# Optimization experiments

Hardware: AMD Instinct MI355X
Metric: run time of the kernel (lower is better)

The kernel has to match this reference:

```python
import jax, jax.numpy as jnp
import numpy as np

N = 50000
E = 800000
IN_F, HID, OUT_F = 512, 256, 64
KEEP = 0.5  # Dropout(0.5)


def setup_inputs() -> dict:
    key = jax.random.key(0)
    ks = jax.random.split(key, 7)
    X = jax.random.normal(ks[0], (N, IN_F), dtype=jnp.float32)
    # Xavier-uniform-style init for the two layer weights
    lim1 = float(np.sqrt(6.0 / (IN_F + HID)))
    lim2 = float(np.sqrt(6.0 / (HID + OUT_F)))
    W1 = jax.random.uniform(ks[1], (IN_F, HID), jnp.float32, -lim1, lim1)
    W2 = jax.random.uniform(ks[2], (HID, OUT_F), jnp.float32, -lim2, lim2)
    a_row = jnp.sort(jax.random.randint(ks[3], (E,), 0, N)).astype(jnp.int64)
    a_col = jax.random.randint(ks[4], (E,), 0, N).astype(jnp.int64)
    a_val = jax.random.uniform(ks[5], (E,), jnp.float32)
    drop_mask = jax.random.randint(ks[6], (N, HID), 0, 2).astype(jnp.int32)
    return {"X": X, "W1": W1, "W2": W2, "a_row": a_row, "a_col": a_col,
            "a_val": a_val, "drop_mask": drop_mask}


def _spmm(a_row, a_col, a_val, dense):
    # A @ dense where A is [N, N] sparse in COO form: gather + weighted segment-sum
    msgs = a_val[:, None] * dense[a_col]          # [E, d]
    return jax.ops.segment_sum(msgs, a_row, num_segments=N)


def reference(X, W1, W2, a_row, a_col, a_val, drop_mask):
    # layer 1: feature transform + neighbor aggregation
    h = _spmm(a_row, a_col, a_val, X @ W1)        # [N, HID]
    h = jax.nn.relu(h)
    h = h * drop_mask.astype(h.dtype) * (1.0 / KEEP)  # Dropout(0.5), train mode
    # layer 2
    out = _spmm(a_row, a_col, a_val, h @ W2)      # [N, OUT_F]
    return jax.nn.log_softmax(out, axis=1)
```

## Files before the change

### kernel.cpp

```cpp
#include <hip/hip_runtime.h>
#include <hip/hip_bf16.h>
#include <math.h>

#define NN   50000
#define EE   800000
#define INF  512
#define HIDF 256
#define OUTF 64
#define MTILES (NN/16)

using short8 = __attribute__((ext_vector_type(8))) short;
using short4v = __attribute__((ext_vector_type(4))) short;
using f32x4  = __attribute__((ext_vector_type(4))) float;

static __device__ __forceinline__ short f2bf(float f){
  unsigned u = __builtin_bit_cast(unsigned, f);
  u += 0x7fff + ((u >> 16) & 1);
  return (short)(u >> 16);
}
static __device__ __forceinline__ float bf2f(short s){
  unsigned u = ((unsigned)(unsigned short)s) << 16;
  return __builtin_bit_cast(float, u);
}

__global__ void k_rowptr(const int* __restrict__ a_row, int* __restrict__ row_ptr){
  int i = blockIdx.x * blockDim.x + threadIdx.x;
  if (i > NN) return;
  int lo = 0, hi = EE;
  while (lo < hi){ int mid = (lo + hi) >> 1; if (a_row[mid] < i) lo = mid + 1; else hi = mid; }
  row_ptr[i] = lo;
}

__global__ void k_pack_w1(const float* __restrict__ W1, short* __restrict__ W1p){
  int idx = blockIdx.x * blockDim.x + threadIdx.x;
  int k = idx >> 8, col = idx & 255;
  int kk = k >> 5, k2 = k & 31;
  W1p[((kk << 8) + col) * 32 + k2] = f2bf(W1[idx]);
}

__global__ void k_transpose_bf16(const float* __restrict__ src, short* __restrict__ dst,
                                 int K, int Ncols){
  int idx = blockIdx.x * blockDim.x + threadIdx.x;
  if (idx >= K * Ncols) return;
  int k = idx / Ncols, n = idx % Ncols;
  dst[n * K + k] = f2bf(src[idx]);
}

__global__ __launch_bounds__(256) void k_gemm1(const float* __restrict__ X,
                                               const short* __restrict__ W1p,
                                               short* __restrict__ XW1b){
  __shared__ short lds[256 * 40];
  int wave = threadIdx.x >> 6, lane = threadIdx.x & 63;
  int l16 = lane & 15, quad = lane >> 4;
  int m0 = blockIdx.x * 64 + wave * 16;
  int arow_idx = min(m0 + l16, NN - 1);
  const float* arow = X + (size_t)arow_idx * INF + quad * 8;

  f32x4 acc[16];
  #pragma unroll
  for (int t = 0; t < 16; t++) acc[t] = (f32x4){0.f,0.f,0.f,0.f};

  for (int kk = 0; kk < INF/32; kk++){
    const short* chunk = W1p + kk * (256*32);
    #pragma unroll
    for (int j = 0; j < 4; j++){
      int off16 = j * 256 + threadIdx.x;
      int col = off16 >> 2, kq = threadIdx.x & 3;
      *(short8*)(lds + col * 40 + kq * 8) = *(const short8*)(chunk + off16 * 8);
    }
    __syncthreads();

    const float4* ap = (const float4*)(arow + kk * 32);
    float4 a0 = ap[0], a1 = ap[1];
    short8 af;
    af[0]=f2bf(a0.x); af[1]=f2bf(a0.y); af[2]=f2bf(a0.z); af[3]=f2bf(a0.w);
    af[4]=f2bf(a1.x); af[5]=f2bf(a1.y); af[6]=f2bf(a1.z); af[7]=f2bf(a1.w);
    #pragma unroll
    for (int nt = 0; nt < 16; nt++){
      short8 bf = *(const short8*)(lds + (nt*16 + l16) * 40 + quad * 8);
      acc[nt] = __builtin_amdgcn_mfma_f32_16x16x32_bf16(af, bf, acc[nt], 0, 0, 0);
    }
    __syncthreads();
  }
  #pragma unroll
  for (int nt = 0; nt < 16; nt++){
    int col = nt*16 + l16;
    #pragma unroll
    for (int r = 0; r < 4; r++){
      int row = m0 + quad*4 + r;
      if (row < NN) XW1b[(size_t)row * HIDF + col] = f2bf(acc[nt][r]);
    }
  }
}

__global__ __launch_bounds__(256) void k_spmm1(const int* __restrict__ row_ptr,
                                               const int* __restrict__ a_col,
                                               const float* __restrict__ a_val,
                                               const short* __restrict__ XW1b,
                                               const int* __restrict__ drop_mask,
                                               short* __restrict__ hb){
  int wave = threadIdx.x >> 6, lane = threadIdx.x & 63;
  int r = blockIdx.x * 4 + wave;
  int s = row_ptr[r], e = row_ptr[r+1];
  int g = lane >> 5;
  int c8 = lane & 31;
  float acc[8] = {0,0,0,0,0,0,0,0};

  for (int i = s + g; i < e; i += 2){
    float v = a_val[i];
    int   c = a_col[i];
    short8 x = *(const short8*)(XW1b + (size_t)c * HIDF + c8 * 8);
    #pragma unroll
    for (int j = 0; j < 8; j++) acc[j] += v * bf2f(x[j]);
  }
  #pragma unroll
  for (int j = 0; j < 8; j++) acc[j] += __shfl_xor(acc[j], 32);

  if (lane < 32){
    int4 d0 = *(const int4*)(drop_mask + (size_t)r * HIDF + c8 * 8);
    int4 d1 = *(const int4*)(drop_mask + (size_t)r * HIDF + c8 * 8 + 4);
    short8 o;
    o[0] = f2bf(fmaxf(acc[0],0.f) * (float)d0.x * 2.0f);
    o[1] = f2bf(fmaxf(acc[1],0.f) * (float)d0.y * 2.0f);
    o[2] = f2bf(fmaxf(acc[2],0.f) * (float)d0.z * 2.0f);
    o[3] = f2bf(fmaxf(acc[3],0.f) * (float)d0.w * 2.0f);
    o[4] = f2bf(fmaxf(acc[4],0.f) * (float)d1.x * 2.0f);
    o[5] = f2bf(fmaxf(acc[5],0.f) * (float)d1.y * 2.0f);
    o[6] = f2bf(fmaxf(acc[6],0.f) * (float)d1.z * 2.0f);
    o[7] = f2bf(fmaxf(acc[7],0.f) * (float)d1.w * 2.0f);
    *(short8*)(hb + (size_t)r * HIDF + c8 * 8) = o;
  }
}

__global__ __launch_bounds__(256) void k_gemm2(const short* __restrict__ A,
                                               const short* __restrict__ BT,
                                               short* __restrict__ C){
  int wave = threadIdx.x >> 6, lane = threadIdx.x & 63;
  int tile_m = blockIdx.x * 4 + wave;
  if (tile_m >= MTILES) return;
  int m0 = tile_m * 16, l16 = lane & 15, quad = lane >> 4;

  f32x4 acc[4];
  #pragma unroll
  for (int t = 0; t < 4; t++) acc[t] = (f32x4){0.f,0.f,0.f,0.f};

  const short* ar = A + (size_t)(m0 + l16) * HIDF + quad * 8;
  for (int kk = 0; kk < HIDF/32; kk++){
    short8 af = *(const short8*)(ar + kk * 32);
    #pragma unroll
    for (int nt = 0; nt < 4; nt++){
      short8 bf = *(const short8*)(BT + (size_t)(nt*16 + l16) * HIDF + kk*32 + quad*8);
      acc[nt] = __builtin_amdgcn_mfma_f32_16x16x32_bf16(af, bf, acc[nt], 0, 0, 0);
    }
  }
  #pragma unroll
  for (int nt = 0; nt < 4; nt++){
    int col = nt*16 + l16;
    #pragma unroll
    for (int r = 0; r < 4; r++)
      C[(size_t)(m0 + quad*4 + r) * OUTF + col] = f2bf(acc[nt][r]);
  }
}

__global__ __launch_bounds__(256) void k_spmm2_lsm(const int* __restrict__ row_ptr,
                                                   const int* __restrict__ a_col,
                                                   const float* __restrict__ a_val,
                                                   const short* __restrict__ HW2b,
                                                   float* __restrict__ out){
  int wave = threadIdx.x >> 6, lane = threadIdx.x & 63;
  int r = blockIdx.x * 4 + wave;
  int s = row_ptr[r], e = row_ptr[r+1];
  int g = lane >> 4;
  int c4 = lane & 15;
  float acc[4] = {0,0,0,0};

  for (int i = s + g; i < e; i += 4){
    float v = a_val[i];
    int   c = a_col[i];
    short4v x = *(const short4v*)(HW2b + (size_t)c * OUTF + c4 * 4);
    #pragma unroll
    for (int j = 0; j < 4; j++) acc[j] += v * bf2f(x[j]);
  }
  #pragma unroll
  for (int j = 0; j < 4; j++){
    acc[j] += __shfl_xor(acc[j], 16);
    acc[j] += __shfl_xor(acc[j], 32);
  }
  float m = fmaxf(fmaxf(acc[0], acc[1]), fmaxf(acc[2], acc[3]));
  #pragma unroll
  for (int o = 1; o <= 8; o <<= 1) m = fmaxf(m, __shfl_xor(m, o));
  float ssum = expf(acc[0]-m) + expf(acc[1]-m) + expf(acc[2]-m) + expf(acc[3]-m);
  #pragma unroll
  for (int o = 1; o <= 8; o <<= 1) ssum += __shfl_xor(ssum, o);
  float ls = logf(ssum);
  if (lane < 16){
    float4 o4 = { acc[0]-m-ls, acc[1]-m-ls, acc[2]-m-ls, acc[3]-m-ls };
    *(float4*)(out + (size_t)r * OUTF + c4 * 4) = o4;
  }
}

extern "C" void kernel_launch(void* const* d_in, const int* in_sizes, int n_in,
                              void* d_out, int out_size, void* d_ws, size_t ws_size,
                              hipStream_t stream) {
  const float* X      = (const float*)d_in[0];
  const float* W1     = (const float*)d_in[1];
  const float* W2     = (const float*)d_in[2];
  const int*   a_row  = (const int*)d_in[3];
  const int*   a_col  = (const int*)d_in[4];
  const float* a_val  = (const float*)d_in[5];
  const int*   drop   = (const int*)d_in[6];
  float*       out    = (float*)d_out;

  char* ws = (char*)d_ws;
  int*   row_ptr = (int*)  (ws);
  short* W1p     = (short*)(ws + 200704);
  short* W2bT    = (short*)(ws + 462848);
  short* XW1b    = (short*)(ws + 495616);
  short* hb      = (short*)(ws + 26095616);
  short* HW2b    = (short*)(ws + 51695616);

  k_rowptr<<<(NN + 1 + 255)/256, 256, 0, stream>>>(a_row, row_ptr);
  k_pack_w1<<<(INF*HIDF)/256, 256, 0, stream>>>(W1, W1p);
  k_transpose_bf16<<<(HIDF*OUTF + 255)/256, 256, 0, stream>>>(W2, W2bT, HIDF, OUTF);
  k_gemm1<<<(NN + 63)/64, 256, 0, stream>>>(X, W1p, XW1b);
  k_spmm1<<<NN/4, 256, 0, stream>>>(row_ptr, a_col, a_val, XW1b, drop, hb);
  k_gemm2<<<(MTILES + 3)/4, 256, 0, stream>>>(hb, W2bT, HW2b);
  k_spmm2_lsm<<<NN/4, 256, 0, stream>>>(row_ptr, a_col, a_val, HW2b, out);
}
```

Baseline: 358.3 us.

## Merge prep kernels, double gemm1 row tile, unroll and widen SpMM gathers

Folds the row-pointer, W1 packing and W2 transpose kernels into a single launch, which removes two kernel launches. gemm1 now has each wave compute two 16-row tiles, so every LDS load of W1 feeds twice as many MFMAs, and the X loads are issued before the barrier. Both SpMM kernels unroll the edge loop by two so more gathers are in flight; spmm1 also moves to 4 edge groups with 16 columns per lane. The cost is higher register pressure in gemm1 (twice the accumulators) and in spmm1 (16 accumulators per lane).

```diff
diff --git a/kernel.cpp b/kernel.cpp
--- a/kernel.cpp
+++ b/kernel.cpp
@@ -23,27 +23,26 @@
   return __builtin_bit_cast(float, u);
 }
 
-__global__ void k_rowptr(const int* __restrict__ a_row, int* __restrict__ row_ptr){
-  int i = blockIdx.x * blockDim.x + threadIdx.x;
-  if (i > NN) return;
-  int lo = 0, hi = EE;
-  while (lo < hi){ int mid = (lo + hi) >> 1; if (a_row[mid] < i) lo = mid + 1; else hi = mid; }
-  row_ptr[i] = lo;
-}
-
-__global__ void k_pack_w1(const float* __restrict__ W1, short* __restrict__ W1p){
-  int idx = blockIdx.x * blockDim.x + threadIdx.x;
-  int k = idx >> 8, col = idx & 255;
-  int kk = k >> 5, k2 = k & 31;
-  W1p[((kk << 8) + col) * 32 + k2] = f2bf(W1[idx]);
-}
-
-__global__ void k_transpose_bf16(const float* __restrict__ src, short* __restrict__ dst,
-                                 int K, int Ncols){
-  int idx = blockIdx.x * blockDim.x + threadIdx.x;
-  if (idx >= K * Ncols) return;
-  int k = idx / Ncols, n = idx % Ncols;
-  dst[n * K + k] = f2bf(src[idx]);
+__global__ void k_prep(const int* __restrict__ a_row, int* __restrict__ row_ptr,
+                       const float* __restrict__ W1, short* __restrict__ W1p,
+                       const float* __restrict__ W2, short* __restrict__ W2bT){
+  int b = blockIdx.x, tid = threadIdx.x;
+  if (b < 196){
+    int i = b * 256 + tid;
+    if (i > NN) return;
+    int lo = 0, hi = EE;
+    while (lo < hi){ int mid = (lo + hi) >> 1; if (a_row[mid] < i) lo = mid + 1; else hi = mid; }
+    row_ptr[i] = lo;
+  } else if (b < 708){
+    int idx = (b - 196) * 256 + tid;
+    int k = idx >> 8, col = idx & 255;
+    int kk = k >> 5, k2 = k & 31;
+    W1p[((kk << 8) + col) * 32 + k2] = f2bf(W1[idx]);
+  } else {
+    int idx = (b - 708) * 256 + tid;
+    int k = idx >> 6, n = idx & 63;
+    W2bT[n * HIDF + k] = f2bf(W2[idx]);
+  }
 }
 
 __global__ __launch_bounds__(256) void k_gemm1(const float* __restrict__ X,
@@ -52,15 +51,22 @@
   __shared__ short lds[256 * 40];
   int wave = threadIdx.x >> 6, lane = threadIdx.x & 63;
   int l16 = lane & 15, quad = lane >> 4;
-  int m0 = blockIdx.x * 64 + wave * 16;
-  int arow_idx = min(m0 + l16, NN - 1);
-  const float* arow = X + (size_t)arow_idx * INF + quad * 8;
-
-  f32x4 acc[16];
-  #pragma unroll
-  for (int t = 0; t < 16; t++) acc[t] = (f32x4){0.f,0.f,0.f,0.f};
+  int m0 = blockIdx.x * 128 + wave * 32;
+  int r0 = min(m0 + l16, NN - 1);
+  int r1 = min(m0 + 16 + l16, NN - 1);
+  const float* arow0 = X + (size_t)r0 * INF + quad * 8;
+  const float* arow1 = X + (size_t)r1 * INF + quad * 8;
+
+  f32x4 acc0[16], acc1[16];
+  #pragma unroll
+  for (int t = 0; t < 16; t++){ acc0[t] = (f32x4){0.f,0.f,0.f,0.f}; acc1[t] = (f32x4){0.f,0.f,0.f,0.f}; }
 
   for (int kk = 0; kk < INF/32; kk++){
+    const float4* ap0 = (const float4*)(arow0 + kk * 32);
+    const float4* ap1 = (const float4*)(arow1 + kk * 32);
+    float4 a00 = ap0[0], a01 = ap0[1];
+    float4 a10 = ap1[0], a11 = ap1[1];
+
     const short* chunk = W1p + kk * (256*32);
     #pragma unroll
     for (int j = 0; j < 4; j++){
@@ -70,15 +76,16 @@
     }
     __syncthreads();
 
-    const float4* ap = (const float4*)(arow + kk * 32);
-    float4 a0 = ap[0], a1 = ap[1];
-    short8 af;
-    af[0]=f2bf(a0.x); af[1]=f2bf(a0.y); af[2]=f2bf(a0.z); af[3]=f2bf(a0.w);
-    af[4]=f2bf(a1.x); af[5]=f2bf(a1.y); af[6]=f2bf(a1.z); af[7]=f2bf(a1.w);
+    short8 af0, af1;
+    af0[0]=f2bf(a00.x); af0[1]=f2bf(a00.y); af0[2]=f2bf(a00.z); af0[3]=f2bf(a00.w);
+    af0[4]=f2bf(a01.x); af0[5]=f2bf(a01.y); af0[6]=f2bf(a01.z); af0[7]=f2bf(a01.w);
+    af1[0]=f2bf(a10.x); af1[1]=f2bf(a10.y); af1[2]=f2bf(a10.z); af1[3]=f2bf(a10.w);
+    af1[4]=f2bf(a11.x); af1[5]=f2bf(a11.y); af1[6]=f2bf(a11.z); af1[7]=f2bf(a11.w);
     #pragma unroll
     for (int nt = 0; nt < 16; nt++){
       short8 bf = *(const short8*)(lds + (nt*16 + l16) * 40 + quad * 8);
-      acc[nt] = __builtin_amdgcn_mfma_f32_16x16x32_bf16(af, bf, acc[nt], 0, 0, 0);
+      acc0[nt] = __builtin_amdgcn_mfma_f32_16x16x32_bf16(af0, bf, acc0[nt], 0, 0, 0);
+      acc1[nt] = __builtin_amdgcn_mfma_f32_16x16x32_bf16(af1, bf, acc1[nt], 0, 0, 0);
     }
     __syncthreads();
   }
@@ -87,8 +94,10 @@
     int col = nt*16 + l16;
     #pragma unroll
     for (int r = 0; r < 4; r++){
-      int row = m0 + quad*4 + r;
-      if (row < NN) XW1b[(size_t)row * HIDF + col] = f2bf(acc[nt][r]);
+      int row0 = m0 + quad*4 + r;
+      int row1 = m0 + 16 + quad*4 + r;
+      if (row0 < NN) XW1b[(size_t)row0 * HIDF + col] = f2bf(acc0[nt][r]);
+      if (row1 < NN) XW1b[(size_t)row1 * HIDF + col] = f2bf(acc1[nt][r]);
     }
   }
 }
@@ -102,33 +111,54 @@
   int wave = threadIdx.x >> 6, lane = threadIdx.x & 63;
   int r = blockIdx.x * 4 + wave;
   int s = row_ptr[r], e = row_ptr[r+1];
-  int g = lane >> 5;
-  int c8 = lane & 31;
-  float acc[8] = {0,0,0,0,0,0,0,0};
-
-  for (int i = s + g; i < e; i += 2){
-    float v = a_val[i];
-    int   c = a_col[i];
-    short8 x = *(const short8*)(XW1b + (size_t)c * HIDF + c8 * 8);
-    #pragma unroll
-    for (int j = 0; j < 8; j++) acc[j] += v * bf2f(x[j]);
-  }
-  #pragma unroll
-  for (int j = 0; j < 8; j++) acc[j] += __shfl_xor(acc[j], 32);
-
-  if (lane < 32){
-    int4 d0 = *(const int4*)(drop_mask + (size_t)r * HIDF + c8 * 8);
-    int4 d1 = *(const int4*)(drop_mask + (size_t)r * HIDF + c8 * 8 + 4);
-    short8 o;
-    o[0] = f2bf(fmaxf(acc[0],0.f) * (float)d0.x * 2.0f);
-    o[1] = f2bf(fmaxf(acc[1],0.f) * (float)d0.y * 2.0f);
-    o[2] = f2bf(fmaxf(acc[2],0.f) * (float)d0.z * 2.0f);
-    o[3] = f2bf(fmaxf(acc[3],0.f) * (float)d0.w * 2.0f);
-    o[4] = f2bf(fmaxf(acc[4],0.f) * (float)d1.x * 2.0f);
-    o[5] = f2bf(fmaxf(acc[5],0.f) * (float)d1.y * 2.0f);
-    o[6] = f2bf(fmaxf(acc[6],0.f) * (float)d1.z * 2.0f);
-    o[7] = f2bf(fmaxf(acc[7],0.f) * (float)d1.w * 2.0f);
-    *(short8*)(hb + (size_t)r * HIDF + c8 * 8) = o;
+  int g = lane >> 4;
+  int c16 = lane & 15;
+  float acc[16];
+  #pragma unroll
+  for (int j = 0; j < 16; j++) acc[j] = 0.f;
+
+  int i = s + g;
+  for (; i + 4 < e; i += 8){
+    float v0 = a_val[i];     int c0 = a_col[i];
+    float v1 = a_val[i+4];   int c1 = a_col[i+4];
+    const short* p0 = XW1b + (size_t)c0 * HIDF + c16 * 16;
+    const short* p1 = XW1b + (size_t)c1 * HIDF + c16 * 16;
+    short8 x0a = *(const short8*)(p0);
+    short8 x0b = *(const short8*)(p0 + 8);
+    short8 x1a = *(const short8*)(p1);
+    short8 x1b = *(const short8*)(p1 + 8);
+    #pragma unroll
+    for (int j = 0; j < 8; j++){
+      acc[j]   += v0 * bf2f(x0a[j]);  acc[j+8] += v0 * bf2f(x0b[j]);
+      acc[j]   += v1 * bf2f(x1a[j]);  acc[j+8] += v1 * bf2f(x1b[j]);
+    }
+  }
+  for (; i < e; i += 4){
+    float v = a_val[i];  int c = a_col[i];
+    const short* p = XW1b + (size_t)c * HIDF + c16 * 16;
+    short8 xa = *(const short8*)(p);
+    short8 xb = *(const short8*)(p + 8);
+    #pragma unroll
+    for (int j = 0; j < 8; j++){
+      acc[j] += v * bf2f(xa[j]);  acc[j+8] += v * bf2f(xb[j]);
+    }
+  }
+  #pragma unroll
+  for (int j = 0; j < 16; j++){
+    acc[j] += __shfl_xor(acc[j], 16);
+    acc[j] += __shfl_xor(acc[j], 32);
+  }
+  if (lane < 16){
+    const int* dm = drop_mask + (size_t)r * HIDF + c16 * 16;
+    short8 o0, o1;
+    #pragma unroll
+    for (int j = 0; j < 8; j++){
+      o0[j] = f2bf(fmaxf(acc[j],   0.f) * (float)dm[j]   * 2.0f);
+      o1[j] = f2bf(fmaxf(acc[j+8], 0.f) * (float)dm[j+8] * 2.0f);
+    }
+    short* hp = hb + (size_t)r * HIDF + c16 * 16;
+    *(short8*)(hp)     = o0;
+    *(short8*)(hp + 8) = o1;
   }
 }
 
@@ -174,9 +204,17 @@
   int c4 = lane & 15;
   float acc[4] = {0,0,0,0};
 
-  for (int i = s + g; i < e; i += 4){
-    float v = a_val[i];
-    int   c = a_col[i];
+  int i = s + g;
+  for (; i + 4 < e; i += 8){
+    float v0 = a_val[i];    int c0 = a_col[i];
+    float v1 = a_val[i+4];  int c1 = a_col[i+4];
+    short4v x0 = *(const short4v*)(HW2b + (size_t)c0 * OUTF + c4 * 4);
+    short4v x1 = *(const short4v*)(HW2b + (size_t)c1 * OUTF + c4 * 4);
+    #pragma unroll
+    for (int j = 0; j < 4; j++){ acc[j] += v0 * bf2f(x0[j]); acc[j] += v1 * bf2f(x1[j]); }
+  }
+  for (; i < e; i += 4){
+    float v = a_val[i];  int c = a_col[i];
     short4v x = *(const short4v*)(HW2b + (size_t)c * OUTF + c4 * 4);
     #pragma unroll
     for (int j = 0; j < 4; j++) acc[j] += v * bf2f(x[j]);
@@ -219,10 +257,8 @@
   short* hb      = (short*)(ws + 26095616);
   short* HW2b    = (short*)(ws + 51695616);
 
-  k_rowptr<<<(NN + 1 + 255)/256, 256, 0, stream>>>(a_row, row_ptr);
-  k_pack_w1<<<(INF*HIDF)/256, 256, 0, stream>>>(W1, W1p);
-  k_transpose_bf16<<<(HIDF*OUTF + 255)/256, 256, 0, stream>>>(W2, W2bT, HIDF, OUTF);
-  k_gemm1<<<(NN + 63)/64, 256, 0, stream>>>(X, W1p, XW1b);
+  k_prep<<<772, 256, 0, stream>>>(a_row, row_ptr, W1, W1p, W2, W2bT);
+  k_gemm1<<<(NN + 127)/128, 256, 0, stream>>>(X, W1p, XW1b);
   k_spmm1<<<NN/4, 256, 0, stream>>>(row_ptr, a_col, a_val, XW1b, drop, hb);
   k_gemm2<<<(MTILES + 3)/4, 256, 0, stream>>>(hb, W2bT, HW2b);
   k_spmm2_lsm<<<NN/4, 256, 0, stream>>>(row_ptr, a_col, a_val, HW2b, out);
```

After: 336.7 us. 1.06x faster.
